# Performance work log

Measured on AMD Instinct MI355X. Metric: run time of the kernel, lower is better.

## Reference

```python
import jax, jax.numpy as jnp
import numpy as np

N = 100000   # nodes
E = 1600000  # edges
F = 128      # input node features
H = 128      # hidden channels
G = 512      # graphs in batch
EPS = 1e-5   # BatchNorm eps


def setup_inputs() -> dict:
    key = jax.random.key(0)
    ks = jax.random.split(key, 24)
    x = jax.random.normal(ks[0], (N, F), jnp.float32)
    edge_index = jax.random.randint(ks[1], (2, E), 0, N)
    batch = jnp.sort(jax.random.randint(ks[2], (N,), 0, G))

    def lin_w(k, i, o):
        return jax.random.normal(k, (i, o), jnp.float32) / np.sqrt(i)

    inp = {
        "x": x, "edge_index": edge_index, "batch": batch,
        "W1": lin_w(ks[3], F, H), "b1": jnp.zeros((H,), jnp.float32),
        "g1": jnp.ones((H,), jnp.float32), "be1": jnp.zeros((H,), jnp.float32),
        "m1": 0.1 * jax.random.normal(ks[4], (H,), jnp.float32),
        "v1": jax.random.uniform(ks[5], (H,), jnp.float32) + 0.5,
        "W2": lin_w(ks[6], H, H), "b2": jnp.zeros((H,), jnp.float32),
        "g2": jnp.ones((H,), jnp.float32), "be2": jnp.zeros((H,), jnp.float32),
        "m2": 0.1 * jax.random.normal(ks[7], (H,), jnp.float32),
        "v2": jax.random.uniform(ks[8], (H,), jnp.float32) + 0.5,
        "W3": lin_w(ks[9], H, H), "b3": jnp.zeros((H,), jnp.float32),
        "g3": jnp.ones((H,), jnp.float32), "be3": jnp.zeros((H,), jnp.float32),
        "m3": 0.1 * jax.random.normal(ks[10], (H,), jnp.float32),
        "v3": jax.random.uniform(ks[11], (H,), jnp.float32) + 0.5,
        "Wl": lin_w(ks[12], H, 1), "bl": jnp.zeros((1,), jnp.float32),
    }
    return inp


def _gcn_norm(edge_index):
    # add self-loops, then symmetric normalization deg^-1/2 A_hat deg^-1/2
    loops = jnp.arange(N)
    src = jnp.concatenate([edge_index[0], loops])
    dst = jnp.concatenate([edge_index[1], loops])
    deg = jax.ops.segment_sum(jnp.ones_like(src, jnp.float32), dst, num_segments=N)
    dinv = jax.lax.rsqrt(jnp.maximum(deg, 1.0))
    norm = dinv[src] * dinv[dst]  # [E+N]
    return src, dst, norm


def _gcn_conv(x, W, b, src, dst, norm):
    h = x @ W                                    # [N,H] dense GEMM first (PyG order)
    msg = h[src] * norm[:, None]                 # gather + scale, [E+N,H]
    agg = jax.ops.segment_sum(msg, dst, num_segments=N)  # scatter-add
    return agg + b


def _bn_relu(x, g, be, m, v):
    # inference BatchNorm1d (running stats) + ReLU
    return jax.nn.relu((x - m) * jax.lax.rsqrt(v + EPS) * g + be)


def reference(x, edge_index, batch,
              W1, b1, g1, be1, m1, v1,
              W2, b2, g2, be2, m2, v2,
              W3, b3, g3, be3, m3, v3,
              Wl, bl):
    src, dst, norm = _gcn_norm(edge_index)
    h = _bn_relu(_gcn_conv(x, W1, b1, src, dst, norm), g1, be1, m1, v1)
    h = _bn_relu(_gcn_conv(h, W2, b2, src, dst, norm), g2, be2, m2, v2)
    h = _bn_relu(_gcn_conv(h, W3, b3, src, dst, norm), g3, be3, m3, v3)
    # global mean pool over graphs
    sums = jax.ops.segment_sum(h, batch, num_segments=G)           # [G,H]
    cnt = jax.ops.segment_sum(jnp.ones((N,), jnp.float32), batch, num_segments=G)
    pooled = sums / jnp.maximum(cnt, 1.0)[:, None]
    # dropout is identity at inference; final linear
    return pooled @ Wl + bl  # [G,1]
```

## Files before the change

### kernel.cpp

```cpp
#include <hip/hip_runtime.h>
#include <hip/hip_bf16.h>

#define NN 100000
#define NE 1600000
#define HD 128
#define NG 512
#define BN_EPS 1e-5f

typedef __attribute__((ext_vector_type(8))) short short8;
typedef __attribute__((ext_vector_type(4))) float floatx4;

__device__ __forceinline__ ushort f2bf(float f) {
    union { float f; uint u; } v; v.f = f;
    uint r = (v.u + 0x7FFF + ((v.u >> 16) & 1)) >> 16;
    return (ushort)r;
}
__device__ __forceinline__ float bflo(uint u) { union { uint u; float f; } v; v.u = u << 16; return v.f; }
__device__ __forceinline__ float bfhi(uint u) { union { uint u; float f; } v; v.u = u & 0xFFFF0000u; return v.f; }

__global__ void k_zero_i(int* p, int n) {
    int i = blockIdx.x * 256 + threadIdx.x;
    if (i < n) p[i] = 0;
}

__global__ void k_hist_rank(const int* __restrict__ dst, int* __restrict__ indeg,
                            int* __restrict__ rank) {
    int e = blockIdx.x * 256 + threadIdx.x;
    if (e < NE) rank[e] = atomicAdd(&indeg[dst[e]], 1);
}

__global__ void k_dinv(const int* __restrict__ indeg, float* __restrict__ dinv) {
    int i = blockIdx.x * 256 + threadIdx.x;
    if (i < NN) dinv[i] = rsqrtf((float)(indeg[i] + 1));
}

__global__ void k_scan1(const int* __restrict__ indeg, int* __restrict__ rs, int* __restrict__ aux) {
    __shared__ int s[256];
    int t = threadIdx.x;
    int base = blockIdx.x * 1024 + t * 4;
    int v0 = 0, v1 = 0, v2 = 0, v3 = 0;
    if (base + 0 < NN) v0 = indeg[base + 0];
    if (base + 1 < NN) v1 = indeg[base + 1];
    if (base + 2 < NN) v2 = indeg[base + 2];
    if (base + 3 < NN) v3 = indeg[base + 3];
    int tsum = v0 + v1 + v2 + v3;
    s[t] = tsum;
    __syncthreads();
    for (int o = 1; o < 256; o <<= 1) {
        int x = 0;
        if (t >= o) x = s[t - o];
        __syncthreads();
        s[t] += x;
        __syncthreads();
    }
    int excl = s[t] - tsum;
    if (base + 0 < NN) rs[base + 0] = excl;
    if (base + 1 < NN) rs[base + 1] = excl + v0;
    if (base + 2 < NN) rs[base + 2] = excl + v0 + v1;
    if (base + 3 < NN) rs[base + 3] = excl + v0 + v1 + v2;
    if (t == 255) aux[blockIdx.x] = s[255];
}

__global__ void k_scan2(int* __restrict__ aux, int nblk) {
    __shared__ int s[128];
    int t = threadIdx.x;
    int v = (t < nblk) ? aux[t] : 0;
    s[t] = v;
    __syncthreads();
    for (int o = 1; o < 128; o <<= 1) {
        int x = 0;
        if (t >= o) x = s[t - o];
        __syncthreads();
        s[t] += x;
        __syncthreads();
    }
    if (t < nblk) aux[t] = s[t] - v;
}

__global__ void k_scan3(int* __restrict__ rs, const int* __restrict__ aux) {
    int i = blockIdx.x * 256 + threadIdx.x;
    if (i < NN) rs[i] += aux[i >> 10];
    if (i == 0) rs[NN] = NE;
}

__global__ void k_fill(const int* __restrict__ src, const int* __restrict__ dst,
                       const int* __restrict__ rank, const int* __restrict__ rs,
                       int* __restrict__ csr) {
    int e = blockIdx.x * 256 + threadIdx.x;
    if (e >= NE) return;
    csr[rs[dst[e]] + rank[e]] = src[e];
}

__global__ void k_bn_prep(const float* __restrict__ b, const float* __restrict__ g,
                          const float* __restrict__ be, const float* __restrict__ m,
                          const float* __restrict__ v, float* scale, float* shift) {
    int f = threadIdx.x;
    if (f < HD) {
        float sc = g[f] * rsqrtf(v[f] + BN_EPS);
        scale[f] = sc;
        shift[f] = (b[f] - m[f]) * sc + be[f];
    }
}

__global__ void k_gstart(const int* __restrict__ batch, int* __restrict__ gstart) {
    int g = blockIdx.x * 256 + threadIdx.x;
    if (g > NG) return;
    if (g == NG) { gstart[NG] = NN; return; }
    int lo = 0, hi = NN;
    while (lo < hi) {
        int mid = (lo + hi) >> 1;
        if (batch[mid] < g) lo = mid + 1; else hi = mid;
    }
    gstart[g] = lo;
}

__global__ void k_cast(const float* __restrict__ x, ushort* __restrict__ xb) {
    long i = (long)(blockIdx.x * 256 + threadIdx.x) * 4;
    if (i >= (long)NN * 128) return;
    float4 v = *(const float4*)(x + i);
    uint2 o;
    o.x = (uint)f2bf(v.x) | ((uint)f2bf(v.y) << 16);
    o.y = (uint)f2bf(v.z) | ((uint)f2bf(v.w) << 16);
    *(uint2*)(xb + i) = o;
}

#define WT_STRIDE 136
__launch_bounds__(256)
__global__ void k_gemm_mfma(const ushort* __restrict__ xb, const float* __restrict__ W,
                            const float* __restrict__ dinv, ushort* __restrict__ hs) {
    __shared__ ushort sWt[128 * WT_STRIDE];
    const int tid = threadIdx.x;
    for (int i = tid; i < 128 * 128; i += 256) {
        int k = i >> 7, n = i & 127;
        sWt[n * WT_STRIDE + k] = f2bf(W[i]);
    }
    __syncthreads();

    const int wave = tid >> 6, lane = tid & 63;
    const int m = lane & 15, kg = lane >> 4;
    const long row0 = (long)blockIdx.x * 64 + wave * 16;

    long arow = row0 + m;
    long arc = arow < NN ? arow : (NN - 1);
    short8 a[4];
#pragma unroll
    for (int s = 0; s < 4; ++s)
        a[s] = *(const short8*)(xb + arc * 128 + s * 32 + kg * 8);

    floatx4 acc[8];
#pragma unroll
    for (int ct = 0; ct < 8; ++ct) acc[ct] = (floatx4){0.f, 0.f, 0.f, 0.f};

#pragma unroll
    for (int s = 0; s < 4; ++s) {
#pragma unroll
        for (int ct = 0; ct < 8; ++ct) {
            short8 b = *(const short8*)&sWt[(ct * 16 + m) * WT_STRIDE + s * 32 + kg * 8];
            acc[ct] = __builtin_amdgcn_mfma_f32_16x16x32_bf16(a[s], b, acc[ct], 0, 0, 0);
        }
    }

#pragma unroll
    for (int r = 0; r < 4; ++r) {
        long orow = row0 + kg * 4 + r;
        if (orow < NN) {
            float dd = dinv[orow];
#pragma unroll
            for (int ct = 0; ct < 8; ++ct)
                hs[orow * 128 + ct * 16 + m] = f2bf(acc[ct][r] * dd);
        }
    }
}

__global__ void k_gather_bf(const ushort* __restrict__ hs, const int* __restrict__ rs,
                            const int* __restrict__ csr, const float* __restrict__ dinv,
                            const float* __restrict__ scale, const float* __restrict__ shift,
                            ushort* __restrict__ xout) {
    int t = blockIdx.x * 256 + threadIdx.x;
    int d = t >> 4;
    if (d >= NN) return;
    int lane = t & 15;
    int c0 = lane * 8;
    int e0 = rs[d], e1 = rs[d + 1];

    uint4 sv = *(const uint4*)(hs + (long)d * 128 + c0);
    float a0 = bflo(sv.x), a1 = bfhi(sv.x), a2 = bflo(sv.y), a3 = bfhi(sv.y);
    float a4 = bflo(sv.z), a5 = bfhi(sv.z), a6 = bflo(sv.w), a7 = bfhi(sv.w);

    int j = e0;
    for (; j + 1 < e1; j += 2) {
        int s0 = csr[j], s1 = csr[j + 1];
        uint4 v0 = *(const uint4*)(hs + (long)s0 * 128 + c0);
        uint4 v1 = *(const uint4*)(hs + (long)s1 * 128 + c0);
        a0 += bflo(v0.x) + bflo(v1.x); a1 += bfhi(v0.x) + bfhi(v1.x);
        a2 += bflo(v0.y) + bflo(v1.y); a3 += bfhi(v0.y) + bfhi(v1.y);
        a4 += bflo(v0.z) + bflo(v1.z); a5 += bfhi(v0.z) + bfhi(v1.z);
        a6 += bflo(v0.w) + bflo(v1.w); a7 += bfhi(v0.w) + bfhi(v1.w);
    }
    if (j < e1) {
        int s0 = csr[j];
        uint4 v0 = *(const uint4*)(hs + (long)s0 * 128 + c0);
        a0 += bflo(v0.x); a1 += bfhi(v0.x);
        a2 += bflo(v0.y); a3 += bfhi(v0.y);
        a4 += bflo(v0.z); a5 += bfhi(v0.z);
        a6 += bflo(v0.w); a7 += bfhi(v0.w);
    }

    float dd = dinv[d];
    float4 sca = *(const float4*)(scale + c0);
    float4 scb = *(const float4*)(scale + c0 + 4);
    float4 sha = *(const float4*)(shift + c0);
    float4 shb = *(const float4*)(shift + c0 + 4);
    float r0 = fmaxf(dd * a0 * sca.x + sha.x, 0.f);
    float r1 = fmaxf(dd * a1 * sca.y + sha.y, 0.f);
    float r2 = fmaxf(dd * a2 * sca.z + sha.z, 0.f);
    float r3 = fmaxf(dd * a3 * sca.w + sha.w, 0.f);
    float r4 = fmaxf(dd * a4 * scb.x + shb.x, 0.f);
    float r5 = fmaxf(dd * a5 * scb.y + shb.y, 0.f);
    float r6 = fmaxf(dd * a6 * scb.z + shb.z, 0.f);
    float r7 = fmaxf(dd * a7 * scb.w + shb.w, 0.f);
    uint4 o;
    o.x = (uint)f2bf(r0) | ((uint)f2bf(r1) << 16);
    o.y = (uint)f2bf(r2) | ((uint)f2bf(r3) << 16);
    o.z = (uint)f2bf(r4) | ((uint)f2bf(r5) << 16);
    o.w = (uint)f2bf(r6) | ((uint)f2bf(r7) << 16);
    *(uint4*)(xout + (long)d * 128 + c0) = o;
}

__global__ void k_pool_final2(const ushort* __restrict__ x, const int* __restrict__ gstart,
                              const float* __restrict__ Wl, const float* __restrict__ bl,
                              float* __restrict__ out) {
    __shared__ float red[256];
    int g = blockIdx.x;
    int tid = threadIdx.x;
    int f = tid & 127;
    int half = tid >> 7;
    int i0 = gstart[g], i1 = gstart[g + 1];

    float acc = 0.f;
    for (int i = i0 + half; i < i1; i += 2) {
        union { uint u; float f; } v; v.u = (uint)x[(long)i * 128 + f] << 16;
        acc += v.f;
    }
    red[tid] = acc;
    __syncthreads();
    if (tid < 128) red[tid] = (red[tid] + red[tid + 128]) * Wl[tid];
    __syncthreads();
    for (int o = 64; o > 0; o >>= 1) {
        if (tid < o) red[tid] += red[tid + o];
        __syncthreads();
    }
    if (tid == 0) out[g] = red[0] / fmaxf((float)(i1 - i0), 1.f) + bl[0];
}

extern "C" void kernel_launch(void* const* d_in, const int* in_sizes, int n_in,
                              void* d_out, int out_size, void* d_ws, size_t ws_size,
                              hipStream_t stream) {
    const float* x   = (const float*)d_in[0];
    const int*   ei  = (const int*)d_in[1];
    const int*   bat = (const int*)d_in[2];
    const float* W1  = (const float*)d_in[3];
    const float* b1  = (const float*)d_in[4];
    const float* g1  = (const float*)d_in[5];
    const float* be1 = (const float*)d_in[6];
    const float* m1  = (const float*)d_in[7];
    const float* v1  = (const float*)d_in[8];
    const float* W2  = (const float*)d_in[9];
    const float* b2  = (const float*)d_in[10];
    const float* g2  = (const float*)d_in[11];
    const float* be2 = (const float*)d_in[12];
    const float* m2  = (const float*)d_in[13];
    const float* v2  = (const float*)d_in[14];
    const float* W3  = (const float*)d_in[15];
    const float* b3  = (const float*)d_in[16];
    const float* g3  = (const float*)d_in[17];
    const float* be3 = (const float*)d_in[18];
    const float* m3  = (const float*)d_in[19];
    const float* v3  = (const float*)d_in[20];
    const float* Wl  = (const float*)d_in[21];
    const float* bl  = (const float*)d_in[22];
    float* out = (float*)d_out;

    const int* srcp = ei;
    const int* dstp = ei + NE;

    char* ws = (char*)d_ws;
    size_t off = 0;
    auto alloc = [&](size_t bytes) { char* p = ws + off; off += (bytes + 255) & ~255ULL; return p; };
    float*  dinv   = (float*) alloc(NN * 4);
    int*    indeg  = (int*)   alloc(NN * 4);
    int*    rs     = (int*)   alloc((NN + 1) * 4);
    int*    aux    = (int*)   alloc(128 * 4);
    int*    csr    = (int*)   alloc(NE * 4);
    int*    rank   = (int*)   alloc(NE * 4);
    float*  scale1 = (float*) alloc(HD * 4);
    float*  shift1 = (float*) alloc(HD * 4);
    float*  scale2 = (float*) alloc(HD * 4);
    float*  shift2 = (float*) alloc(HD * 4);
    float*  scale3 = (float*) alloc(HD * 4);
    float*  shift3 = (float*) alloc(HD * 4);
    int*    gstart = (int*)   alloc((NG + 1) * 4);
    ushort* xb     = (ushort*)alloc((size_t)NN * HD * 2);
    ushort* hs     = (ushort*)alloc((size_t)NN * HD * 2);
    ushort* xbuf   = (ushort*)alloc((size_t)NN * HD * 2);

    const int nblk_scan = (NN + 1023) / 1024;
    const int grid_n    = (NN + 255) / 256;
    const int grid_e    = (NE + 255) / 256;
    const int gemm_grid = (NN + 63) / 64;
    const int gath_grid = (NN * 16 + 255) / 256;
    const int cast_grid = (NN * 128 / 4 + 255) / 256;

    k_zero_i<<<grid_n, 256, 0, stream>>>(indeg, NN);
    k_hist_rank<<<grid_e, 256, 0, stream>>>(dstp, indeg, rank);
    k_dinv<<<grid_n, 256, 0, stream>>>(indeg, dinv);
    k_scan1<<<nblk_scan, 256, 0, stream>>>(indeg, rs, aux);
    k_scan2<<<1, 128, 0, stream>>>(aux, nblk_scan);
    k_scan3<<<grid_n, 256, 0, stream>>>(rs, aux);
    k_fill<<<grid_e, 256, 0, stream>>>(srcp, dstp, rank, rs, csr);

    k_bn_prep<<<1, 128, 0, stream>>>(b1, g1, be1, m1, v1, scale1, shift1);
    k_bn_prep<<<1, 128, 0, stream>>>(b2, g2, be2, m2, v2, scale2, shift2);
    k_bn_prep<<<1, 128, 0, stream>>>(b3, g3, be3, m3, v3, scale3, shift3);
    k_gstart<<<3, 256, 0, stream>>>(bat, gstart);
    k_cast<<<cast_grid, 256, 0, stream>>>(x, xb);

    k_gemm_mfma<<<gemm_grid, 256, 0, stream>>>(xb, W1, dinv, hs);
    k_gather_bf<<<gath_grid, 256, 0, stream>>>(hs, rs, csr, dinv, scale1, shift1, xbuf);
    k_gemm_mfma<<<gemm_grid, 256, 0, stream>>>(xbuf, W2, dinv, hs);
    k_gather_bf<<<gath_grid, 256, 0, stream>>>(hs, rs, csr, dinv, scale2, shift2, xbuf);
    k_gemm_mfma<<<gemm_grid, 256, 0, stream>>>(xbuf, W3, dinv, hs);
    k_gather_bf<<<gath_grid, 256, 0, stream>>>(hs, rs, csr, dinv, scale3, shift3, xbuf);

    k_pool_final2<<<NG, 256, 0, stream>>>(xbuf, gstart, Wl, bl, out);
}
```

Before: 524.8 us.

## Fuse layer-1 GEMM with degree histogram and pre-transpose weights once

The layer-1 GEMM now reads fp32 x directly and converts to bf16 in registers, which removes the separate cast kernel. It runs in the same launch as the in-degree histogram, using extra blocks, so the two proceed concurrently. Because dinv is not yet known at that point, layer 1 applies the source-side dinv scaling inside the gather, at the cost of an extra dinv load per edge. Weights are converted and transposed to bf16 once by a prep kernel so the later GEMMs copy them with vector loads, and the dinv computation and BN-prep launches are merged into existing or single kernels.

```diff
diff --git a/kernel.cpp b/kernel.cpp
--- a/kernel.cpp
+++ b/kernel.cpp
@@ -7,6 +7,9 @@
 #define NG 512
 #define BN_EPS 1e-5f
 
+#define GEMM_BLOCKS 1563
+#define HIST_BLOCKS 6250
+
 typedef __attribute__((ext_vector_type(8))) short short8;
 typedef __attribute__((ext_vector_type(4))) float floatx4;
 
@@ -23,18 +26,75 @@
     if (i < n) p[i] = 0;
 }
 
-__global__ void k_hist_rank(const int* __restrict__ dst, int* __restrict__ indeg,
-                            int* __restrict__ rank) {
-    int e = blockIdx.x * 256 + threadIdx.x;
-    if (e < NE) rank[e] = atomicAdd(&indeg[dst[e]], 1);
-}
-
-__global__ void k_dinv(const int* __restrict__ indeg, float* __restrict__ dinv) {
-    int i = blockIdx.x * 256 + threadIdx.x;
-    if (i < NN) dinv[i] = rsqrtf((float)(indeg[i] + 1));
-}
-
-__global__ void k_scan1(const int* __restrict__ indeg, int* __restrict__ rs, int* __restrict__ aux) {
+__global__ void k_prep_w3(const float* __restrict__ W1, const float* __restrict__ W2,
+                          const float* __restrict__ W3,
+                          ushort* __restrict__ Wt1, ushort* __restrict__ Wt2,
+                          ushort* __restrict__ Wt3) {
+    int w = blockIdx.x >> 6;
+    int i = (blockIdx.x & 63) * 256 + threadIdx.x;
+    const float* W = (w == 0) ? W1 : (w == 1) ? W2 : W3;
+    ushort* Wt = (w == 0) ? Wt1 : (w == 1) ? Wt2 : Wt3;
+    int k = i >> 7, n = i & 127;
+    Wt[n * 128 + k] = f2bf(W[i]);
+}
+
+__launch_bounds__(256)
+__global__ void k_fused1(const float* __restrict__ x, const ushort* __restrict__ Wt,
+                         ushort* __restrict__ hs,
+                         const int* __restrict__ dst, int* __restrict__ indeg,
+                         int* __restrict__ rank) {
+    const int tid = threadIdx.x;
+    if (blockIdx.x >= GEMM_BLOCKS) {
+        int e = (blockIdx.x - GEMM_BLOCKS) * 256 + tid;
+        if (e < NE) rank[e] = atomicAdd(&indeg[dst[e]], 1);
+        return;
+    }
+    const int wave = tid >> 6, lane = tid & 63;
+    const int m = lane & 15, kg = lane >> 4;
+    const long row0 = (long)blockIdx.x * 64 + wave * 16;
+
+    long arow = row0 + m;
+    long arc = arow < NN ? arow : (NN - 1);
+    const float* xf = x + arc * 128;
+    short8 a[4];
+#pragma unroll
+    for (int s = 0; s < 4; ++s) {
+        float4 f0 = *(const float4*)(xf + s * 32 + kg * 8);
+        float4 f1 = *(const float4*)(xf + s * 32 + kg * 8 + 4);
+        short8 t;
+        t[0] = (short)f2bf(f0.x); t[1] = (short)f2bf(f0.y);
+        t[2] = (short)f2bf(f0.z); t[3] = (short)f2bf(f0.w);
+        t[4] = (short)f2bf(f1.x); t[5] = (short)f2bf(f1.y);
+        t[6] = (short)f2bf(f1.z); t[7] = (short)f2bf(f1.w);
+        a[s] = t;
+    }
+
+    floatx4 acc[8];
+#pragma unroll
+    for (int ct = 0; ct < 8; ++ct) acc[ct] = (floatx4){0.f, 0.f, 0.f, 0.f};
+
+#pragma unroll
+    for (int s = 0; s < 4; ++s) {
+#pragma unroll
+        for (int ct = 0; ct < 8; ++ct) {
+            short8 b = *(const short8*)(Wt + (ct * 16 + m) * 128 + s * 32 + kg * 8);
+            acc[ct] = __builtin_amdgcn_mfma_f32_16x16x32_bf16(a[s], b, acc[ct], 0, 0, 0);
+        }
+    }
+
+#pragma unroll
+    for (int r = 0; r < 4; ++r) {
+        long orow = row0 + kg * 4 + r;
+        if (orow < NN) {
+#pragma unroll
+            for (int ct = 0; ct < 8; ++ct)
+                hs[orow * 128 + ct * 16 + m] = f2bf(acc[ct][r]);
+        }
+    }
+}
+
+__global__ void k_scan1d(const int* __restrict__ indeg, int* __restrict__ rs,
+                         int* __restrict__ aux, float* __restrict__ dinv) {
     __shared__ int s[256];
     int t = threadIdx.x;
     int base = blockIdx.x * 1024 + t * 4;
@@ -43,6 +103,10 @@
     if (base + 1 < NN) v1 = indeg[base + 1];
     if (base + 2 < NN) v2 = indeg[base + 2];
     if (base + 3 < NN) v3 = indeg[base + 3];
+    if (base + 0 < NN) dinv[base + 0] = rsqrtf((float)(v0 + 1));
+    if (base + 1 < NN) dinv[base + 1] = rsqrtf((float)(v1 + 1));
+    if (base + 2 < NN) dinv[base + 2] = rsqrtf((float)(v2 + 1));
+    if (base + 3 < NN) dinv[base + 3] = rsqrtf((float)(v3 + 1));
     int tsum = v0 + v1 + v2 + v3;
     s[t] = tsum;
     __syncthreads();
@@ -91,15 +155,26 @@
     csr[rs[dst[e]] + rank[e]] = src[e];
 }
 
-__global__ void k_bn_prep(const float* __restrict__ b, const float* __restrict__ g,
-                          const float* __restrict__ be, const float* __restrict__ m,
-                          const float* __restrict__ v, float* scale, float* shift) {
-    int f = threadIdx.x;
-    if (f < HD) {
-        float sc = g[f] * rsqrtf(v[f] + BN_EPS);
-        scale[f] = sc;
-        shift[f] = (b[f] - m[f]) * sc + be[f];
-    }
+__global__ void k_bn_prep3(const float* __restrict__ b1, const float* __restrict__ g1,
+                           const float* __restrict__ be1, const float* __restrict__ m1,
+                           const float* __restrict__ v1,
+                           const float* __restrict__ b2, const float* __restrict__ g2,
+                           const float* __restrict__ be2, const float* __restrict__ m2,
+                           const float* __restrict__ v2,
+                           const float* __restrict__ b3, const float* __restrict__ g3,
+                           const float* __restrict__ be3, const float* __restrict__ m3,
+                           const float* __restrict__ v3,
+                           float* scale1, float* shift1, float* scale2, float* shift2,
+                           float* scale3, float* shift3) {
+    int l = blockIdx.x, f = threadIdx.x;
+    const float *b, *g, *be, *m, *v;
+    float *sc, *sh;
+    if (l == 0)      { b = b1; g = g1; be = be1; m = m1; v = v1; sc = scale1; sh = shift1; }
+    else if (l == 1) { b = b2; g = g2; be = be2; m = m2; v = v2; sc = scale2; sh = shift2; }
+    else             { b = b3; g = g3; be = be3; m = m3; v = v3; sc = scale3; sh = shift3; }
+    float s = g[f] * rsqrtf(v[f] + BN_EPS);
+    sc[f] = s;
+    sh[f] = (b[f] - m[f]) * s + be[f];
 }
 
 __global__ void k_gstart(const int* __restrict__ batch, int* __restrict__ gstart) {
@@ -114,25 +189,15 @@
     gstart[g] = lo;
 }
 
-__global__ void k_cast(const float* __restrict__ x, ushort* __restrict__ xb) {
-    long i = (long)(blockIdx.x * 256 + threadIdx.x) * 4;
-    if (i >= (long)NN * 128) return;
-    float4 v = *(const float4*)(x + i);
-    uint2 o;
-    o.x = (uint)f2bf(v.x) | ((uint)f2bf(v.y) << 16);
-    o.y = (uint)f2bf(v.z) | ((uint)f2bf(v.w) << 16);
-    *(uint2*)(xb + i) = o;
-}
-
 #define WT_STRIDE 136
 __launch_bounds__(256)
-__global__ void k_gemm_mfma(const ushort* __restrict__ xb, const float* __restrict__ W,
-                            const float* __restrict__ dinv, ushort* __restrict__ hs) {
+__global__ void k_gemm_l23(const ushort* __restrict__ xb, const ushort* __restrict__ Wt,
+                           const float* __restrict__ dinv, ushort* __restrict__ hs) {
     __shared__ ushort sWt[128 * WT_STRIDE];
     const int tid = threadIdx.x;
-    for (int i = tid; i < 128 * 128; i += 256) {
-        int k = i >> 7, n = i & 127;
-        sWt[n * WT_STRIDE + k] = f2bf(W[i]);
+    for (int i = tid; i < 2048; i += 256) {
+        int row = i >> 4, seg = i & 15;
+        *(uint4*)&sWt[row * WT_STRIDE + seg * 8] = *(const uint4*)(Wt + row * 128 + seg * 8);
     }
     __syncthreads();
 
@@ -172,6 +237,7 @@
     }
 }
 
+template <bool SCALE_SRC>
 __global__ void k_gather_bf(const ushort* __restrict__ hs, const int* __restrict__ rs,
                             const int* __restrict__ csr, const float* __restrict__ dinv,
                             const float* __restrict__ scale, const float* __restrict__ shift,
@@ -182,31 +248,45 @@
     int lane = t & 15;
     int c0 = lane * 8;
     int e0 = rs[d], e1 = rs[d + 1];
+    float dd = dinv[d];
 
     uint4 sv = *(const uint4*)(hs + (long)d * 128 + c0);
-    float a0 = bflo(sv.x), a1 = bfhi(sv.x), a2 = bflo(sv.y), a3 = bfhi(sv.y);
-    float a4 = bflo(sv.z), a5 = bfhi(sv.z), a6 = bflo(sv.w), a7 = bfhi(sv.w);
+    float w = SCALE_SRC ? dd : 1.0f;
+    float a0 = w * bflo(sv.x), a1 = w * bfhi(sv.x), a2 = w * bflo(sv.y), a3 = w * bfhi(sv.y);
+    float a4 = w * bflo(sv.z), a5 = w * bfhi(sv.z), a6 = w * bflo(sv.w), a7 = w * bfhi(sv.w);
 
     int j = e0;
     for (; j + 1 < e1; j += 2) {
         int s0 = csr[j], s1 = csr[j + 1];
         uint4 v0 = *(const uint4*)(hs + (long)s0 * 128 + c0);
         uint4 v1 = *(const uint4*)(hs + (long)s1 * 128 + c0);
-        a0 += bflo(v0.x) + bflo(v1.x); a1 += bfhi(v0.x) + bfhi(v1.x);
-        a2 += bflo(v0.y) + bflo(v1.y); a3 += bfhi(v0.y) + bfhi(v1.y);
-        a4 += bflo(v0.z) + bflo(v1.z); a5 += bfhi(v0.z) + bfhi(v1.z);
-        a6 += bflo(v0.w) + bflo(v1.w); a7 += bfhi(v0.w) + bfhi(v1.w);
+        if (SCALE_SRC) {
+            float w0 = dinv[s0], w1 = dinv[s1];
+            a0 += w0 * bflo(v0.x) + w1 * bflo(v1.x);
+            a1 += w0 * bfhi(v0.x) + w1 * bfhi(v1.x);
+            a2 += w0 * bflo(v0.y) + w1 * bflo(v1.y);
+            a3 += w0 * bfhi(v0.y) + w1 * bfhi(v1.y);
+            a4 += w0 * bflo(v0.z) + w1 * bflo(v1.z);
+            a5 += w0 * bfhi(v0.z) + w1 * bfhi(v1.z);
+            a6 += w0 * bflo(v0.w) + w1 * bflo(v1.w);
+            a7 += w0 * bfhi(v0.w) + w1 * bfhi(v1.w);
+        } else {
+            a0 += bflo(v0.x) + bflo(v1.x); a1 += bfhi(v0.x) + bfhi(v1.x);
+            a2 += bflo(v0.y) + bflo(v1.y); a3 += bfhi(v0.y) + bfhi(v1.y);
+            a4 += bflo(v0.z) + bflo(v1.z); a5 += bfhi(v0.z) + bfhi(v1.z);
+            a6 += bflo(v0.w) + bflo(v1.w); a7 += bfhi(v0.w) + bfhi(v1.w);
+        }
     }
     if (j < e1) {
         int s0 = csr[j];
         uint4 v0 = *(const uint4*)(hs + (long)s0 * 128 + c0);
-        a0 += bflo(v0.x); a1 += bfhi(v0.x);
-        a2 += bflo(v0.y); a3 += bfhi(v0.y);
-        a4 += bflo(v0.z); a5 += bfhi(v0.z);
-        a6 += bflo(v0.w); a7 += bfhi(v0.w);
-    }
-
-    float dd = dinv[d];
+        float w0 = SCALE_SRC ? dinv[s0] : 1.0f;
+        a0 += w0 * bflo(v0.x); a1 += w0 * bfhi(v0.x);
+        a2 += w0 * bflo(v0.y); a3 += w0 * bfhi(v0.y);
+        a4 += w0 * bflo(v0.z); a5 += w0 * bfhi(v0.z);
+        a6 += w0 * bflo(v0.w); a7 += w0 * bfhi(v0.w);
+    }
+
     float4 sca = *(const float4*)(scale + c0);
     float4 scb = *(const float4*)(scale + c0 + 4);
     float4 sha = *(const float4*)(shift + c0);
@@ -300,37 +380,37 @@
     float*  scale3 = (float*) alloc(HD * 4);
     float*  shift3 = (float*) alloc(HD * 4);
     int*    gstart = (int*)   alloc((NG + 1) * 4);
-    ushort* xb     = (ushort*)alloc((size_t)NN * HD * 2);
+    ushort* Wt1    = (ushort*)alloc(128 * 128 * 2);
+    ushort* Wt2    = (ushort*)alloc(128 * 128 * 2);
+    ushort* Wt3    = (ushort*)alloc(128 * 128 * 2);
     ushort* hs     = (ushort*)alloc((size_t)NN * HD * 2);
     ushort* xbuf   = (ushort*)alloc((size_t)NN * HD * 2);
 
     const int nblk_scan = (NN + 1023) / 1024;
     const int grid_n    = (NN + 255) / 256;
     const int grid_e    = (NE + 255) / 256;
-    const int gemm_grid = (NN + 63) / 64;
     const int gath_grid = (NN * 16 + 255) / 256;
-    const int cast_grid = (NN * 128 / 4 + 255) / 256;
 
     k_zero_i<<<grid_n, 256, 0, stream>>>(indeg, NN);
-    k_hist_rank<<<grid_e, 256, 0, stream>>>(dstp, indeg, rank);
-    k_dinv<<<grid_n, 256, 0, stream>>>(indeg, dinv);
-    k_scan1<<<nblk_scan, 256, 0, stream>>>(indeg, rs, aux);
+    k_prep_w3<<<192, 256, 0, stream>>>(W1, W2, W3, Wt1, Wt2, Wt3);
+
+    k_fused1<<<GEMM_BLOCKS + HIST_BLOCKS, 256, 0, stream>>>(x, Wt1, hs, dstp, indeg, rank);
+
+    k_scan1d<<<nblk_scan, 256, 0, stream>>>(indeg, rs, aux, dinv);
     k_scan2<<<1, 128, 0, stream>>>(aux, nblk_scan);
     k_scan3<<<grid_n, 256, 0, stream>>>(rs, aux);
     k_fill<<<grid_e, 256, 0, stream>>>(srcp, dstp, rank, rs, csr);
 
-    k_bn_prep<<<1, 128, 0, stream>>>(b1, g1, be1, m1, v1, scale1, shift1);
-    k_bn_prep<<<1, 128, 0, stream>>>(b2, g2, be2, m2, v2, scale2, shift2);
-    k_bn_prep<<<1, 128, 0, stream>>>(b3, g3, be3, m3, v3, scale3, shift3);
+    k_bn_prep3<<<3, 128, 0, stream>>>(b1, g1, be1, m1, v1, b2, g2, be2, m2, v2,
+                                      b3, g3, be3, m3, v3,
+                                      scale1, shift1, scale2, shift2, scale3, shift3);
     k_gstart<<<3, 256, 0, stream>>>(bat, gstart);
-    k_cast<<<cast_grid, 256, 0, stream>>>(x, xb);
-
-    k_gemm_mfma<<<gemm_grid, 256, 0, stream>>>(xb, W1, dinv, hs);
-    k_gather_bf<<<gath_grid, 256, 0, stream>>>(hs, rs, csr, dinv, scale1, shift1, xbuf);
-    k_gemm_mfma<<<gemm_grid, 256, 0, stream>>>(xbuf, W2, dinv, hs);
-    k_gather_bf<<<gath_grid, 256, 0, stream>>>(hs, rs, csr, dinv, scale2, shift2, xbuf);
-    k_gemm_mfma<<<gemm_grid, 256, 0, stream>>>(xbuf, W3, dinv, hs);
-    k_gather_bf<<<gath_grid, 256, 0, stream>>>(hs, rs, csr, dinv, scale3, shift3, xbuf);
+
+    k_gather_bf<true><<<gath_grid, 256, 0, stream>>>(hs, rs, csr, dinv, scale1, shift1, xbuf);
+    k_gemm_l23<<<GEMM_BLOCKS, 256, 0, stream>>>(xbuf, Wt2, dinv, hs);
+    k_gather_bf<false><<<gath_grid, 256, 0, stream>>>(hs, rs, csr, dinv, scale2, shift2, xbuf);
+    k_gemm_l23<<<GEMM_BLOCKS, 256, 0, stream>>>(xbuf, Wt3, dinv, hs);
+    k_gather_bf<false><<<gath_grid, 256, 0, stream>>>(hs, rs, csr, dinv, scale3, shift3, xbuf);
 
     k_pool_final2<<<NG, 256, 0, stream>>>(xbuf, gstart, Wl, bl, out);
 }
```

Result: faster. 508.1 us (-3.2%).
